# Performance work log

Hardware: AMD Instinct MI355X
Metric: run time of the kernel (lower is better)

Reference implementation:

```python
import jax, jax.numpy as jnp
import numpy as np

PD = 256            # pretrain_dim == dim_in (standard mode)
DZ = 128            # dim_z
PD2 = PD + 2        # feature dim after concatenating 2-d coords
FD = PD + 2 * PD2   # final_dim = 772
TEMP = float(DZ) ** 0.5
EPS = 1e-12
N1, N2 = 4096, 2048


def _lin_init(key, din, dout):
    w = jax.random.normal(key, (dout, din), jnp.float32) * 0.02
    b = jnp.zeros((dout,), jnp.float32)
    return w, b


def _lin(x, w, b):
    return x @ w.T + b


def setup_inputs() -> dict:
    key = jax.random.key(0)
    ks = jax.random.split(key, 13)
    lm_X = jax.random.normal(ks[0], (N1, PD), jnp.float32)
    lm_Y = jax.random.normal(ks[1], (N1, 2), jnp.float32)
    tg_X = jax.random.normal(ks[2], (N2, PD), jnp.float32)
    tg_Y = jax.random.normal(ks[3], (N2, 2), jnp.float32)
    lm_delay = jax.random.uniform(ks[4], (N1,), jnp.float32)
    tg_delay = jax.random.uniform(ks[5], (N2,), jnp.float32)
    aq_w, aq_b = _lin_init(ks[6], PD, DZ)    # att_attribute q proj
    ak_w, ak_b = _lin_init(ks[7], PD, DZ)    # att_attribute k proj
    w1_w, w1_b = _lin_init(ks[8], PD2, PD2)  # self.w_1
    w2_w, w2_b = _lin_init(ks[9], PD2, PD2)  # self.w_2
    pq_w, pq_b = _lin_init(ks[10], FD, DZ)   # pred attention q proj
    pk_w, pk_b = _lin_init(ks[11], PD, DZ)   # pred attention k proj
    pv_w, pv_b = _lin_init(ks[12], 2, 2)     # pred attention v proj
    gamma1 = jnp.ones((1, 1), jnp.float32)
    gamma2 = jnp.ones((1, 1), jnp.float32)
    gamma3 = jnp.ones((1, 1), jnp.float32)
    alpha = jnp.ones((1, 1), jnp.float32)
    beta = jnp.zeros((1, 1), jnp.float32)
    return dict(lm_X=lm_X, lm_Y=lm_Y, tg_X=tg_X, tg_Y=tg_Y,
                lm_delay=lm_delay, tg_delay=tg_delay,
                aq_w=aq_w, aq_b=aq_b, ak_w=ak_w, ak_b=ak_b,
                w1_w=w1_w, w1_b=w1_b, w2_w=w2_w, w2_b=w2_b,
                pq_w=pq_w, pq_b=pq_b, pk_w=pk_w, pk_b=pk_b,
                pv_w=pv_w, pv_b=pv_b,
                gamma1=gamma1, gamma2=gamma2, gamma3=gamma3,
                alpha=alpha, beta=beta)


def reference(lm_X, lm_Y, tg_X, tg_Y, lm_delay, tg_delay,
              aq_w, aq_b, ak_w, ak_b,
              w1_w, w1_b, w2_w, w2_b,
              pq_w, pq_b, pk_w, pk_b, pv_w, pv_b,
              gamma1, gamma2, gamma3, alpha, beta):
    n2 = tg_X.shape[0]
    a = alpha[0, 0]
    b0 = beta[0, 0]

    lm_feature = jnp.concatenate([lm_X, lm_Y], axis=1)            # [N1, PD2]
    tg_feature_0 = jnp.concatenate([tg_X, jnp.zeros((n2, 2), lm_X.dtype)], axis=1)
    router_0 = jnp.mean(lm_feature, axis=0)                        # [PD2]

    delay_score = jnp.exp(-gamma1[0, 0] * (a * lm_delay + b0))     # [N1]
    rou0 = jnp.exp(-gamma2[0, 0] * (a * tg_delay + b0))            # [N2]
    rou1 = jnp.exp(-gamma3[0, 0] * (a * tg_delay + b0))            # [N2]

    # SimpleAttention1: attribute score of targets over landmarks
    q = _lin(tg_X, aq_w, aq_b)
    k = _lin(lm_X, ak_w, ak_b)
    attr = jnp.exp(jax.nn.softmax((q / TEMP) @ k.T, axis=-1))      # [N2, N1]

    # Degree-normalized propagation of adj_matrix_0 (block-structured:
    # lm rows = identity, tg rows = [attr | I | rou0-col], router row = [delay | 0 | 1]).
    deg_tg0 = 1.0 + attr.sum(axis=1) + rou0                        # [N2]
    tg_prop0 = (attr @ lm_feature + tg_feature_0 + rou0[:, None] * router_0[None, :]) \
               / (deg_tg0 + EPS)[:, None]
    router_prop0 = (delay_score @ lm_feature + router_0) / (1.0 + delay_score.sum() + EPS)

    tg_feature_1 = _lin(tg_prop0, w1_w, w1_b)                      # [N2, PD2]
    router_1 = _lin(router_prop0[None, :], w1_w, w1_b)             # [1, PD2]

    # Second propagation: adj_matrix_1 = I + rou1 on tg->router column.
    tg_prop1 = (tg_feature_1 + rou1[:, None] * router_1) / (1.0 + rou1 + EPS)[:, None]
    tg_feature_2 = _lin(tg_prop1, w2_w, w2_b)                      # [N2, PD2]

    final_tg_feature = jnp.concatenate([tg_X, tg_feature_1, tg_feature_2], axis=-1)  # [N2, FD]

    # SimpleAttention2 (collaborative MLP prediction)
    q2 = _lin(final_tg_feature, pq_w, pq_b)
    k2 = _lin(lm_X, pk_w, pk_b)
    v2 = _lin(lm_Y, pv_w, pv_b)
    attn2 = jax.nn.softmax((q2 / TEMP) @ k2.T, axis=-1)            # [N2, N1]
    y_pred = attn2 @ v2                                            # [N2, 2]
    return y_pred, final_tg_feature
```

## Files before the change

kernel.cpp:

```cpp
#include <hip/hip_runtime.h>

#define N1 4096
#define N2 2048
#define PD 256
#define DZ 128
#define PD2 258
#define PD2P 264
#define FD 772
#define FDP 776
#define APN 272
#define APLD 72
#define SPLITS 16

typedef short s8v __attribute__((ext_vector_type(8)));
typedef float f32x4 __attribute__((ext_vector_type(4)));

__device__ __forceinline__ short f2b(float f) {
    union { float f; unsigned u; } v; v.f = f;
    unsigned r = v.u + 0x7fffu + ((v.u >> 16) & 1u);
    return (short)(r >> 16);
}
__device__ __forceinline__ float sb2f(short s) {
    union { unsigned u; float f; } v;
    v.u = ((unsigned)(unsigned short)s) << 16;
    return v.f;
}

constexpr int R0 = N2 * PD;
constexpr int R1 = R0 + PD2 * PD2P;
constexpr int R2 = R1 + PD2 * PD2P;
constexpr int R3 = R2 + DZ * FDP;
constexpr int R4 = R3 + APN * N1;
constexpr int R5 = R4 + 4096;
constexpr int R6 = R5 + 2048;
constexpr int R7 = R6 + N2 * 4;
constexpr int R8 = R7 + N2 * 6;

__global__ __launch_bounds__(256) void cvt_all(
    const float* __restrict__ lmX, const float* __restrict__ lmY,
    const float* __restrict__ tgX,
    const float* __restrict__ pqw, const float* __restrict__ w1w,
    const float* __restrict__ w2w,
    const float* __restrict__ lmd, const float* __restrict__ tgd,
    const float* __restrict__ g1, const float* __restrict__ g2,
    const float* __restrict__ g3, const float* __restrict__ al,
    const float* __restrict__ be,
    const float* __restrict__ pvw, const float* __restrict__ pvb,
    short* __restrict__ w1wb, short* __restrict__ w2wb,
    short* __restrict__ pqwb, short* __restrict__ lmFTb,
    float* __restrict__ dscore, float* __restrict__ rou0,
    float* __restrict__ rou1, float* __restrict__ v2b,
    float* __restrict__ Z, short* __restrict__ finalFb,
    short* __restrict__ tgp1b, float* __restrict__ outF)
{
    int i = blockIdx.x * 256 + threadIdx.x;
    if (i < R0) { int r = i >> 8, c = i & 255;
                  float v = tgX[i];
                  outF[(size_t)r * FD + c] = v;
                  finalFb[(size_t)r * FDP + c] = f2b(v); return; }
    if (i < R1) { int j = i - R0; int r = j / PD2P, c = j - r * PD2P;
                  w1wb[j] = (c < PD2) ? f2b(w1w[r * PD2 + c]) : (short)0; return; }
    if (i < R2) { int j = i - R1; int r = j / PD2P, c = j - r * PD2P;
                  w2wb[j] = (c < PD2) ? f2b(w2w[r * PD2 + c]) : (short)0; return; }
    if (i < R3) { int j = i - R2; int r = j / FDP, c = j - r * FDP;
                  pqwb[j] = (c < FD) ? f2b(pqw[r * FD + c]) : (short)0; return; }
    if (i < R4) { int j = i - R3; int c = j >> 12, r = j & (N1 - 1);
                  float v = 0.f;
                  if (c < PD) v = lmX[(size_t)r * PD + c];
                  else if (c < PD2) v = lmY[r * 2 + (c - PD)];
                  else if (c == PD2) v = 1.0f;
                  lmFTb[j] = f2b(v); return; }
    if (i < R5) { int j = i - R4;
                  float a = al[0], b = be[0];
                  dscore[j] = __expf(-g1[0] * (a * lmd[j] + b));
                  float y0 = lmY[2 * j], y1 = lmY[2 * j + 1];
                  v2b[2 * j]     = pvw[0] * y0 + pvw[1] * y1 + pvb[0];
                  v2b[2 * j + 1] = pvw[2] * y0 + pvw[3] * y1 + pvb[1];
                  if (j < N2) { float t = a * tgd[j] + b;
                                rou0[j] = __expf(-g2[0] * t);
                                rou1[j] = __expf(-g3[0] * t); }
                  return; }
    if (i < R6) { Z[i - R5] = 0.f; return; }
    if (i < R7) { int j = i - R6; int r = j >> 2;
                  finalFb[(size_t)r * FDP + FD + (j & 3)] = 0; return; }
    if (i < R8) { int j = i - R7; int r = j / 6;
                  tgp1b[(size_t)r * PD2P + PD2 + (j - r * 6)] = 0; return; }
}

__global__ __launch_bounds__(256) void rkq_kernel(
    const float* __restrict__ lmX, const float* __restrict__ tgX,
    const float* __restrict__ aqw, const float* __restrict__ aqb,
    const float* __restrict__ akw, const float* __restrict__ akb,
    const float* __restrict__ pkw, const float* __restrict__ pkb,
    const short* __restrict__ lmFTb, const float* __restrict__ dscore,
    float* __restrict__ router0, float* __restrict__ routerp0,
    short* __restrict__ kk, short* __restrict__ qb)
{
    __shared__ __align__(16) short LDS[5120];
    const int j = blockIdx.x, tid = threadIdx.x;
    const int lane = tid & 63, wv = tid >> 6;
    const int wm = wv >> 1, wn = wv & 1;
    const int lm = lane & 15, lq = lane >> 4;
    const f32x4 zero4 = {0.f, 0.f, 0.f, 0.f};

    if (j < 258) {
        float* r1 = (float*)LDS;
        float* r2 = r1 + 256;
        float* r3 = r2 + 256;
        const short* rowp = lmFTb + (size_t)j * N1;
        float s1 = 0.f, s2 = 0.f, s3 = 0.f;
        for (int i = tid; i < N1; i += 256) {
            float v = sb2f(rowp[i]);
            float d = dscore[i];
            s1 += v; s2 += d * v; s3 += d;
        }
        r1[tid] = s1; r2[tid] = s2; r3[tid] = s3; __syncthreads();
        for (int o = 128; o > 0; o >>= 1) {
            if (tid < o) { r1[tid] += r1[tid + o]; r2[tid] += r2[tid + o]; r3[tid] += r3[tid + o]; }
            __syncthreads();
        }
        if (tid == 0) {
            float r0v = r1[0] / (float)N1;
            router0[j] = r0v;
            routerp0[j] = (r2[0] + r0v) / (1.f + r3[0] + 1e-12f);
        }
        return;
    }
    short* Als = LDS;
    short* Bls = LDS + 64 * 40;
    f32x4 acc[2][2] = {{zero4, zero4}, {zero4, zero4}};
    const int r = tid >> 2, cgp = tid & 3;
    if (j < 514) {
        int jt = j - 258;
        int row0 = (jt >> 2) * 64, col0 = (jt & 3) * 64;
        for (int k0 = 0; k0 < 256; k0 += 32) {
            int gk = k0 + cgp * 8;
            const float* ap = lmX + (size_t)(row0 + r) * PD + gk;
            int c = col0 + r;
            const float* bp = (c < 128) ? akw + (size_t)c * PD + gk
                                        : pkw + (size_t)(c - 128) * PD + gk;
            s8v va, vb;
#pragma unroll
            for (int q = 0; q < 8; ++q) { va[q] = f2b(ap[q]); vb[q] = f2b(bp[q]); }
            *(s8v*)(Als + r * 40 + cgp * 8) = va;
            *(s8v*)(Bls + r * 40 + cgp * 8) = vb;
            __syncthreads();
            s8v af[2], bf[2];
#pragma unroll
            for (int mt = 0; mt < 2; ++mt)
                af[mt] = *(const s8v*)(Als + (wm * 32 + mt * 16 + lm) * 40 + lq * 8);
#pragma unroll
            for (int nt = 0; nt < 2; ++nt)
                bf[nt] = *(const s8v*)(Bls + (wn * 32 + nt * 16 + lm) * 40 + lq * 8);
#pragma unroll
            for (int mt = 0; mt < 2; ++mt)
#pragma unroll
                for (int nt = 0; nt < 2; ++nt)
                    acc[mt][nt] = __builtin_amdgcn_mfma_f32_16x16x32_bf16(
                        af[mt], bf[nt], acc[mt][nt], 0, 0, 0);
            __syncthreads();
        }
#pragma unroll
        for (int mt = 0; mt < 2; ++mt)
#pragma unroll
            for (int nt = 0; nt < 2; ++nt) {
                int c = col0 + wn * 32 + nt * 16 + lm;
                float bv = (c < 128) ? akb[c] : pkb[c - 128];
#pragma unroll
                for (int i = 0; i < 4; ++i) {
                    int rr = row0 + wm * 32 + mt * 16 + lq * 4 + i;
                    kk[(size_t)rr * 256 + c] = f2b(acc[mt][nt][i] + bv);
                }
            }
    } else {
        int jt = j - 514;
        int row0 = (jt >> 1) * 64, col0 = (jt & 1) * 64;
        for (int k0 = 0; k0 < 256; k0 += 32) {
            int gk = k0 + cgp * 8;
            const float* ap = tgX + (size_t)(row0 + r) * PD + gk;
            const float* bp = aqw + (size_t)(col0 + r) * PD + gk;
            s8v va, vb;
#pragma unroll
            for (int q = 0; q < 8; ++q) { va[q] = f2b(ap[q]); vb[q] = f2b(bp[q]); }
            *(s8v*)(Als + r * 40 + cgp * 8) = va;
            *(s8v*)(Bls + r * 40 + cgp * 8) = vb;
            __syncthreads();
            s8v af[2], bf[2];
#pragma unroll
            for (int mt = 0; mt < 2; ++mt)
                af[mt] = *(const s8v*)(Als + (wm * 32 + mt * 16 + lm) * 40 + lq * 8);
#pragma unroll
            for (int nt = 0; nt < 2; ++nt)
                bf[nt] = *(const s8v*)(Bls + (wn * 32 + nt * 16 + lm) * 40 + lq * 8);
#pragma unroll
            for (int mt = 0; mt < 2; ++mt)
#pragma unroll
                for (int nt = 0; nt < 2; ++nt)
                    acc[mt][nt] = __builtin_amdgcn_mfma_f32_16x16x32_bf16(
                        af[mt], bf[nt], acc[mt][nt], 0, 0, 0);
            __syncthreads();
        }
        const float INV_TEMP = 0.08838834764831845f;
#pragma unroll
        for (int mt = 0; mt < 2; ++mt)
#pragma unroll
            for (int nt = 0; nt < 2; ++nt) {
                int c = col0 + wn * 32 + nt * 16 + lm;
                float bv = aqb[c];
#pragma unroll
                for (int i = 0; i < 4; ++i) {
                    int rr = row0 + wm * 32 + mt * 16 + lq * 4 + i;
                    qb[(size_t)rr * DZ + c] = f2b(INV_TEMP * (acc[mt][nt][i] + bv));
                }
            }
    }
}

__global__ __launch_bounds__(256) void scores_e(
    const short* __restrict__ Q, const short* __restrict__ Kk,
    short* __restrict__ E, float* __restrict__ Z,
    const float* __restrict__ rp0, const float* __restrict__ w1w,
    const float* __restrict__ w1b, float* __restrict__ router1)
{
    const int j = blockIdx.x, tid = threadIdx.x;
    if (j == 512) {
        for (int c = tid; c < PD2; c += 256) {
            float s = w1b[c];
            const float* wr = w1w + (size_t)c * PD2;
            for (int k = 0; k < PD2; ++k) s += rp0[k] * wr[k];
            router1[c] = s;
        }
        return;
    }
    __shared__ __align__(16) short LDS[10240];
    short* Als = LDS;
    short* Bls = LDS + 128 * 40;
    const int lane = tid & 63, wv = tid >> 6;
    const int wm = wv >> 1, wn = wv & 1;
    const int lm = lane & 15, lq = lane >> 4;
    const int row0 = (j >> 5) * 128, col0 = (j & 31) * 128;
    const f32x4 zero4 = {0.f, 0.f, 0.f, 0.f};
    f32x4 acc[4][4];
#pragma unroll
    for (int mt = 0; mt < 4; ++mt)
#pragma unroll
        for (int nt = 0; nt < 4; ++nt) acc[mt][nt] = zero4;
    for (int k0 = 0; k0 < 128; k0 += 32) {
#pragma unroll
        for (int l = 0; l < 2; ++l) {
            int id = l * 256 + tid;
            int r = id >> 2, cgp = id & 3;
            int gk = k0 + cgp * 8;
            *(s8v*)(Als + r * 40 + cgp * 8) = *(const s8v*)(Q + (size_t)(row0 + r) * DZ + gk);
            *(s8v*)(Bls + r * 40 + cgp * 8) = *(const s8v*)(Kk + (size_t)(col0 + r) * 256 + gk);
        }
        __syncthreads();
        s8v af[4], bf[4];
#pragma unroll
        for (int mt = 0; mt < 4; ++mt)
            af[mt] = *(const s8v*)(Als + (wm * 64 + mt * 16 + lm) * 40 + lq * 8);
#pragma unroll
        for (int nt = 0; nt < 4; ++nt)
            bf[nt] = *(const s8v*)(Bls + (wn * 64 + nt * 16 + lm) * 40 + lq * 8);
#pragma unroll
        for (int mt = 0; mt < 4; ++mt)
#pragma unroll
            for (int nt = 0; nt < 4; ++nt)
                acc[mt][nt] = __builtin_amdgcn_mfma_f32_16x16x32_bf16(
                    af[mt], bf[nt], acc[mt][nt], 0, 0, 0);
        __syncthreads();
    }
#pragma unroll
    for (int mt = 0; mt < 4; ++mt)
#pragma unroll
        for (int i = 0; i < 4; ++i) {
            int r = row0 + wm * 64 + mt * 16 + lq * 4 + i;
            float rs = 0.f;
#pragma unroll
            for (int nt = 0; nt < 4; ++nt) {
                int c = col0 + wn * 64 + nt * 16 + lm;
                float e = __expf(acc[mt][nt][i]);
                E[(size_t)r * N1 + c] = f2b(e);
                rs += e;
            }
#pragma unroll
            for (int msk = 1; msk < 16; msk <<= 1) rs += __shfl_xor(rs, msk, 64);
            if (lm == 0) atomicAdd(&Z[r], rs);
        }
}

__global__ __launch_bounds__(512) void ap_gemm(const short* __restrict__ E,
                                               const float* __restrict__ Z,
                                               const short* __restrict__ lmFTb,
                                               short* __restrict__ part)
{
    __shared__ __align__(16) short LDS[28800];
    const int tid = threadIdx.x, bid = blockIdx.x;
    const int lane = tid & 63, w8 = tid >> 6;
    const int lm = lane & 15, lq = lane >> 4;
    const int s = bid & 15, row0 = (bid >> 4) * 128;
    const int kbase = s * (N1 / SPLITS);
    short* Als = LDS;
    short* Bls = LDS + 128 * APLD;
    const f32x4 zero4 = {0.f, 0.f, 0.f, 0.f};
    f32x4 acc[17];
#pragma unroll
    for (int nt = 0; nt < 17; ++nt) acc[nt] = zero4;
    for (int it = 0; it < (N1 / SPLITS) / 64; ++it) {
        int k0 = kbase + it * 64;
#pragma unroll
        for (int l = 0; l < 2; ++l) {
            int id = l * 512 + tid;
            int r = id >> 3, gg = id & 7;
            s8v ev = *(const s8v*)(E + (size_t)(row0 + r) * N1 + k0 + gg * 8);
            float invZ = __builtin_amdgcn_rcpf(Z[row0 + r]);
            s8v av;
#pragma unroll
            for (int q = 0; q < 8; ++q)
                av[q] = f2b(__expf(sb2f(ev[q]) * invZ));
            *(s8v*)(Als + r * APLD + gg * 8) = av;
        }
#pragma unroll
        for (int l = 0; l < 5; ++l) {
            int id = l * 512 + tid;
            if (id < APN * 8) {
                int r = id >> 3, gg = id & 7;
                *(s8v*)(Bls + r * APLD + gg * 8) =
                    *(const s8v*)(lmFTb + (size_t)r * N1 + k0 + gg * 8);
            }
        }
        __syncthreads();
        s8v a0 = *(const s8v*)(Als + (w8 * 16 + lm) * APLD + lq * 8);
        s8v a1 = *(const s8v*)(Als + (w8 * 16 + lm) * APLD + 32 + lq * 8);
#pragma unroll
        for (int nt = 0; nt < 17; ++nt) {
            s8v b0 = *(const s8v*)(Bls + (nt * 16 + lm) * APLD + lq * 8);
            s8v b1 = *(const s8v*)(Bls + (nt * 16 + lm) * APLD + 32 + lq * 8);
            acc[nt] = __builtin_amdgcn_mfma_f32_16x16x32_bf16(a0, b0, acc[nt], 0, 0, 0);
            acc[nt] = __builtin_amdgcn_mfma_f32_16x16x32_bf16(a1, b1, acc[nt], 0, 0, 0);
        }
        __syncthreads();
    }
    short* op = part + (size_t)s * N2 * APN;
#pragma unroll
    for (int nt = 0; nt < 17; ++nt) {
        int c = nt * 16 + lm;
#pragma unroll
        for (int i = 0; i < 4; ++i) {
            int r = row0 + w8 * 16 + lq * 4 + i;
            op[(size_t)r * APN + c] = f2b(acc[nt][i]);
        }
    }
}

__global__ __launch_bounds__(256) void fix_tgp0(const short* __restrict__ part,
                                                const float* __restrict__ tgX,
                                                const float* __restrict__ rou0,
                                                const float* __restrict__ router0,
                                                short* __restrict__ outb) {
    int r = blockIdx.x;
    int tid = threadIdx.x;
    __shared__ float sAsum;
    float s0 = 0.f, s1 = 0.f;
#pragma unroll
    for (int s = 0; s < SPLITS; ++s)
        s0 += sb2f(part[((size_t)s * N2 + r) * APN + tid]);
    if (tid < 8) {
#pragma unroll
        for (int s = 0; s < SPLITS; ++s)
            s1 += sb2f(part[((size_t)s * N2 + r) * APN + 256 + tid]);
    }
    if (tid == 2) sAsum = s1;
    __syncthreads();
    float ro = rou0[r];
    float inv = 1.f / (1.f + sAsum + ro + 1e-12f);
    {
        float v = (s0 + tgX[(size_t)r * PD + tid] + ro * router0[tid]) * inv;
        outb[(size_t)r * PD2P + tid] = f2b(v);
    }
    if (tid < 8) {
        int c = 256 + tid;
        float v = 0.f;
        if (c < PD2) v = (s1 + ro * router0[c]) * inv;
        outb[(size_t)r * PD2P + c] = f2b(v);
    }
}

__global__ __launch_bounds__(256) void w_gemm(
    const short* __restrict__ A, const short* __restrict__ B,
    const float* __restrict__ bias,
    float* __restrict__ outFcol, short* __restrict__ fFbcol,
    const float* __restrict__ rou1, const float* __restrict__ router1,
    short* __restrict__ tgp1b)
{
    __shared__ __align__(16) short LDS[5120];
    short* Als = LDS;
    short* Bls = LDS + 64 * 40;
    const int tid = threadIdx.x;
    const int lane = tid & 63, wv = tid >> 6;
    const int wm = wv >> 1, wn = wv & 1;
    const int lm = lane & 15, lq = lane >> 4;
    const int row0 = blockIdx.y * 64, col0 = blockIdx.x * 64;
    const f32x4 zero4 = {0.f, 0.f, 0.f, 0.f};
    f32x4 acc[2][2] = {{zero4, zero4}, {zero4, zero4}};
    const s8v zero8 = {0, 0, 0, 0, 0, 0, 0, 0};
    const int r = tid >> 2, cgp = tid & 3;
    for (int k0 = 0; k0 < PD2P; k0 += 32) {
        int gk = k0 + cgp * 8;
        s8v va = zero8, vb = zero8;
        if (gk < PD2P) {
            va = *(const s8v*)(A + (size_t)(row0 + r) * PD2P + gk);
            if (col0 + r < PD2) vb = *(const s8v*)(B + (size_t)(col0 + r) * PD2P + gk);
        }
        *(s8v*)(Als + r * 40 + cgp * 8) = va;
        *(s8v*)(Bls + r * 40 + cgp * 8) = vb;
        __syncthreads();
        s8v af[2], bf[2];
#pragma unroll
        for (int mt = 0; mt < 2; ++mt)
            af[mt] = *(const s8v*)(Als + (wm * 32 + mt * 16 + lm) * 40 + lq * 8);
#pragma unroll
        for (int nt = 0; nt < 2; ++nt)
            bf[nt] = *(const s8v*)(Bls + (wn * 32 + nt * 16 + lm) * 40 + lq * 8);
#pragma unroll
        for (int mt = 0; mt < 2; ++mt)
#pragma unroll
            for (int nt = 0; nt < 2; ++nt)
                acc[mt][nt] = __builtin_amdgcn_mfma_f32_16x16x32_bf16(
                    af[mt], bf[nt], acc[mt][nt], 0, 0, 0);
        __syncthreads();
    }
#pragma unroll
    for (int mt = 0; mt < 2; ++mt)
#pragma unroll
        for (int nt = 0; nt < 2; ++nt) {
            int c = col0 + wn * 32 + nt * 16 + lm;
            if (c >= PD2) continue;
            float bv = bias[c];
            float rc = router1 ? router1[c] : 0.f;
#pragma unroll
            for (int i = 0; i < 4; ++i) {
                int rr = row0 + wm * 32 + mt * 16 + lq * 4 + i;
                float v = acc[mt][nt][i] + bv;
                outFcol[(size_t)rr * FD + c] = v;
                fFbcol[(size_t)rr * FDP + c] = f2b(v);
                if (tgp1b) {
                    float ro = rou1[rr];
                    tgp1b[(size_t)rr * PD2P + c] =
                        f2b((v + ro * rc) / (1.f + ro + 1e-12f));
                }
            }
        }
}

__global__ __launch_bounds__(256) void q2_gemm(
    const short* __restrict__ A, const short* __restrict__ B,
    const float* __restrict__ bias, short* __restrict__ outB)
{
    __shared__ __align__(16) short LDS[5120];
    short* Als = LDS;
    short* Bls = LDS + 64 * 40;
    const int tid = threadIdx.x;
    const int lane = tid & 63, wv = tid >> 6;
    const int wm = wv >> 1, wn = wv & 1;
    const int lm = lane & 15, lq = lane >> 4;
    const int row0 = blockIdx.y * 64, col0 = blockIdx.x * 64;
    const f32x4 zero4 = {0.f, 0.f, 0.f, 0.f};
    f32x4 acc[2][2] = {{zero4, zero4}, {zero4, zero4}};
    const s8v zero8 = {0, 0, 0, 0, 0, 0, 0, 0};
    const int r = tid >> 2, cgp = tid & 3;
    for (int k0 = 0; k0 < FDP; k0 += 32) {
        int gk = k0 + cgp * 8;
        s8v va = zero8, vb = zero8;
        if (gk < FDP) {
            va = *(const s8v*)(A + (size_t)(row0 + r) * FDP + gk);
            vb = *(const s8v*)(B + (size_t)(col0 + r) * FDP + gk);
        }
        *(s8v*)(Als + r * 40 + cgp * 8) = va;
        *(s8v*)(Bls + r * 40 + cgp * 8) = vb;
        __syncthreads();
        s8v af[2], bf[2];
#pragma unroll
        for (int mt = 0; mt < 2; ++mt)
            af[mt] = *(const s8v*)(Als + (wm * 32 + mt * 16 + lm) * 40 + lq * 8);
#pragma unroll
        for (int nt = 0; nt < 2; ++nt)
            bf[nt] = *(const s8v*)(Bls + (wn * 32 + nt * 16 + lm) * 40 + lq * 8);
#pragma unroll
        for (int mt = 0; mt < 2; ++mt)
#pragma unroll
            for (int nt = 0; nt < 2; ++nt)
                acc[mt][nt] = __builtin_amdgcn_mfma_f32_16x16x32_bf16(
                    af[mt], bf[nt], acc[mt][nt], 0, 0, 0);
        __syncthreads();
    }
    const float INV_TEMP = 0.08838834764831845f;
#pragma unroll
    for (int mt = 0; mt < 2; ++mt)
#pragma unroll
        for (int nt = 0; nt < 2; ++nt) {
            int c = col0 + wn * 32 + nt * 16 + lm;
            float bv = bias[c];
#pragma unroll
            for (int i = 0; i < 4; ++i) {
                int rr = row0 + wm * 32 + mt * 16 + lq * 4 + i;
                outB[(size_t)rr * DZ + c] = f2b(INV_TEMP * (acc[mt][nt][i] + bv));
            }
        }
}

__global__ __launch_bounds__(256) void attn2_flash(
    const short* __restrict__ Q, const short* __restrict__ Kk,
    const float* __restrict__ V, float* __restrict__ part2,
    unsigned* __restrict__ done, float* __restrict__ out)
{
    __shared__ __align__(16) short Qls[64 * 136];
    __shared__ __align__(16) short Kls[64 * 136];
    __shared__ float Vls[128];
    __shared__ unsigned sdone;
    const int tid = threadIdx.x;
    const int lane = tid & 63, wv = tid >> 6;
    const int lm = lane & 15, lq = lane >> 4;
    const int chunk = blockIdx.x & 7, row0 = (blockIdx.x >> 3) * 64;
    const f32x4 zero4 = {0.f, 0.f, 0.f, 0.f};
#pragma unroll
    for (int l = 0; l < 4; ++l) {
        int id = l * 256 + tid;
        int r = id >> 4, g = id & 15;
        *(s8v*)(Qls + r * 136 + g * 8) = *(const s8v*)(Q + (size_t)(row0 + r) * DZ + g * 8);
    }
    __syncthreads();
    s8v af[4];
#pragma unroll
    for (int ks = 0; ks < 4; ++ks)
        af[ks] = *(const s8v*)(Qls + (wv * 16 + lm) * 136 + ks * 32 + lq * 8);
    float z[4] = {0.f, 0.f, 0.f, 0.f};
    float y0[4] = {0.f, 0.f, 0.f, 0.f};
    float y1[4] = {0.f, 0.f, 0.f, 0.f};
    for (int t = 0; t < 8; ++t) {
        int col0 = chunk * 512 + t * 64;
        __syncthreads();
#pragma unroll
        for (int l = 0; l < 4; ++l) {
            int id = l * 256 + tid;
            int r = id >> 4, g = id & 15;
            *(s8v*)(Kls + r * 136 + g * 8) =
                *(const s8v*)(Kk + (size_t)(col0 + r) * 256 + 128 + g * 8);
        }
        if (tid < 128) Vls[tid] = V[col0 * 2 + tid];
        __syncthreads();
        f32x4 acc[4];
#pragma unroll
        for (int nt = 0; nt < 4; ++nt) acc[nt] = zero4;
#pragma unroll
        for (int nt = 0; nt < 4; ++nt)
#pragma unroll
            for (int ks = 0; ks < 4; ++ks) {
                s8v bf = *(const s8v*)(Kls + (nt * 16 + lm) * 136 + ks * 32 + lq * 8);
                acc[nt] = __builtin_amdgcn_mfma_f32_16x16x32_bf16(af[ks], bf, acc[nt], 0, 0, 0);
            }
        float v0[4], v1[4];
#pragma unroll
        for (int nt = 0; nt < 4; ++nt) {
            v0[nt] = Vls[(nt * 16 + lm) * 2];
            v1[nt] = Vls[(nt * 16 + lm) * 2 + 1];
        }
#pragma unroll
        for (int i = 0; i < 4; ++i) {
            float e0 = __expf(acc[0][i]), e1 = __expf(acc[1][i]);
            float e2 = __expf(acc[2][i]), e3 = __expf(acc[3][i]);
            float pz = e0 + e1 + e2 + e3;
            float py0 = e0 * v0[0] + e1 * v0[1] + e2 * v0[2] + e3 * v0[3];
            float py1 = e0 * v1[0] + e1 * v1[1] + e2 * v1[2] + e3 * v1[3];
#pragma unroll
            for (int msk = 1; msk < 16; msk <<= 1) {
                pz  += __shfl_xor(pz, msk, 64);
                py0 += __shfl_xor(py0, msk, 64);
                py1 += __shfl_xor(py1, msk, 64);
            }
            z[i] += pz; y0[i] += py0; y1[i] += py1;
        }
    }
    if (lm == 0) {
#pragma unroll
        for (int i = 0; i < 4; ++i) {
            int r = row0 + wv * 16 + lq * 4 + i;
            float* pp = part2 + ((size_t)r * 8 + chunk) * 4;
            pp[0] = z[i]; pp[1] = y0[i]; pp[2] = y1[i];
        }
    }
    __threadfence();
    __syncthreads();
    if (tid == 0) sdone = atomicAdd(done, 1u);
    __syncthreads();
    if (sdone == 255u) {
        __threadfence();
        for (int r = tid; r < N2; r += 256) {
            const float* pp = part2 + (size_t)r * 32;
            float Zt = 0.f, Y0 = 0.f, Y1 = 0.f;
#pragma unroll
            for (int c = 0; c < 8; ++c) {
                Zt += pp[c * 4]; Y0 += pp[c * 4 + 1]; Y1 += pp[c * 4 + 2];
            }
            out[2 * r] = Y0 / Zt;
            out[2 * r + 1] = Y1 / Zt;
        }
    }
}

extern "C" void kernel_launch(void* const* d_in, const int* in_sizes, int n_in,
                              void* d_out, int out_size, void* d_ws, size_t ws_size,
                              hipStream_t stream) {
    const float* lm_X = (const float*)d_in[0];
    const float* lm_Y = (const float*)d_in[1];
    const float* tg_X = (const float*)d_in[2];
    const float* lm_delay = (const float*)d_in[4];
    const float* tg_delay = (const float*)d_in[5];
    const float* aq_w = (const float*)d_in[6];
    const float* aq_b = (const float*)d_in[7];
    const float* ak_w = (const float*)d_in[8];
    const float* ak_b = (const float*)d_in[9];
    const float* w1_w = (const float*)d_in[10];
    const float* w1_b = (const float*)d_in[11];
    const float* w2_w = (const float*)d_in[12];
    const float* w2_b = (const float*)d_in[13];
    const float* pq_w = (const float*)d_in[14];
    const float* pq_b = (const float*)d_in[15];
    const float* pk_w = (const float*)d_in[16];
    const float* pk_b = (const float*)d_in[17];
    const float* pv_w = (const float*)d_in[18];
    const float* pv_b = (const float*)d_in[19];
    const float* g1 = (const float*)d_in[20];
    const float* g2 = (const float*)d_in[21];
    const float* g3 = (const float*)d_in[22];
    const float* al = (const float*)d_in[23];
    const float* be = (const float*)d_in[24];

    float* out = (float*)d_out;
    float* outF = out + (size_t)N2 * 2;

    char* base = (char*)d_ws;
    size_t off = 0;
    auto allocF = [&](size_t n) -> float* {
        float* q = (float*)(base + off);
        off += (n * 4 + 255) / 256 * 256;
        return q;
    };
    auto allocS = [&](size_t n) -> short* {
        short* q = (short*)(base + off);
        off += (n * 2 + 255) / 256 * 256;
        return q;
    };

    short* E        = allocS((size_t)N2 * N1);
    short* appart   = allocS((size_t)SPLITS * N2 * APN);
    short* lmFTb    = allocS((size_t)APN * N1);
    short* qb       = allocS((size_t)N2 * DZ);
    short* kk       = allocS((size_t)N1 * 256);
    short* q2       = allocS((size_t)N2 * DZ);
    short* tgp0b    = allocS((size_t)N2 * PD2P);
    short* tgp1b    = allocS((size_t)N2 * PD2P);
    short* finalFb  = allocS((size_t)N2 * FDP);
    short* w1wb     = allocS((size_t)PD2 * PD2P);
    short* w2wb     = allocS((size_t)PD2 * PD2P);
    short* pqwb     = allocS((size_t)DZ * FDP);
    float* v2b      = allocF((size_t)N1 * 2);
    float* part2    = allocF((size_t)N2 * 32);
    float* Zbuf     = allocF(N2);
    float* router0  = allocF(PD2);
    float* routerp0 = allocF(PD2);
    float* router1  = allocF(PD2);
    float* dscore   = allocF(N1);
    float* rou0     = allocF(N2);
    float* rou1     = allocF(N2);
    unsigned* done  = (unsigned*)allocF(64);

    hipMemsetAsync(done, 0, 256, stream);

    hipLaunchKernelGGL(cvt_all, dim3((R8 + 255) / 256), dim3(256), 0, stream,
                       lm_X, lm_Y, tg_X, pq_w, w1_w, w2_w,
                       lm_delay, tg_delay, g1, g2, g3, al, be, pv_w, pv_b,
                       w1wb, w2wb, pqwb, lmFTb,
                       dscore, rou0, rou1, v2b, Zbuf, finalFb, tgp1b, outF);
    hipLaunchKernelGGL(rkq_kernel, dim3(578), dim3(256), 0, stream,
                       lm_X, tg_X, aq_w, aq_b, ak_w, ak_b, pk_w, pk_b,
                       lmFTb, dscore, router0, routerp0, kk, qb);
    hipLaunchKernelGGL(scores_e, dim3(513), dim3(256), 0, stream,
                       qb, kk, E, Zbuf, routerp0, w1_w, w1_b, router1);
    hipLaunchKernelGGL(ap_gemm, dim3(256), dim3(512), 0, stream, E, Zbuf, lmFTb, appart);
    hipLaunchKernelGGL(fix_tgp0, dim3(N2), dim3(256), 0, stream,
                       appart, tg_X, rou0, router0, tgp0b);
    hipLaunchKernelGGL(w_gemm, dim3(5, 32), dim3(256), 0, stream,
                       tgp0b, w1wb, w1_b, outF + 256, finalFb + 256, rou1, router1, tgp1b);
    hipLaunchKernelGGL(w_gemm, dim3(5, 32), dim3(256), 0, stream,
                       tgp1b, w2wb, w2_b, outF + 514, finalFb + 514,
                       nullptr, nullptr, nullptr);
    hipLaunchKernelGGL(q2_gemm, dim3(2, 32), dim3(256), 0, stream,
                       finalFb, pqwb, pq_b, q2);
    hipLaunchKernelGGL(attn2_flash, dim3(256), dim3(256), 0, stream,
                       q2, kk, v2b, part2, done, out);
}
```

Before: 253.5 us.

## Split attn2 across more column chunks and move combine to separate kernel

Doubles the column splits in the final attention from 8 to 16, launching 512 blocks that each cover 256 key columns, which raises occupancy on the GPU. The per-tile cross-lane shuffle reductions are deferred to a single reduction after the loop. The last-block atomic counter, threadfence and memset are replaced by a separate small combine kernel. This adds one kernel launch and doubles the partial-results buffer.

```diff
diff --git a/kernel.cpp b/kernel.cpp
--- a/kernel.cpp
+++ b/kernel.cpp
@@ -511,17 +511,15 @@
 
 __global__ __launch_bounds__(256) void attn2_flash(
     const short* __restrict__ Q, const short* __restrict__ Kk,
-    const float* __restrict__ V, float* __restrict__ part2,
-    unsigned* __restrict__ done, float* __restrict__ out)
+    const float* __restrict__ V, float* __restrict__ part2)
 {
     __shared__ __align__(16) short Qls[64 * 136];
     __shared__ __align__(16) short Kls[64 * 136];
     __shared__ float Vls[128];
-    __shared__ unsigned sdone;
     const int tid = threadIdx.x;
     const int lane = tid & 63, wv = tid >> 6;
     const int lm = lane & 15, lq = lane >> 4;
-    const int chunk = blockIdx.x & 7, row0 = (blockIdx.x >> 3) * 64;
+    const int chunk = blockIdx.x & 15, row0 = (blockIdx.x >> 4) * 64;
     const f32x4 zero4 = {0.f, 0.f, 0.f, 0.f};
 #pragma unroll
     for (int l = 0; l < 4; ++l) {
@@ -537,8 +535,8 @@
     float z[4] = {0.f, 0.f, 0.f, 0.f};
     float y0[4] = {0.f, 0.f, 0.f, 0.f};
     float y1[4] = {0.f, 0.f, 0.f, 0.f};
-    for (int t = 0; t < 8; ++t) {
-        int col0 = chunk * 512 + t * 64;
+    for (int t = 0; t < 4; ++t) {
+        int col0 = chunk * 256 + t * 64;
         __syncthreads();
 #pragma unroll
         for (int l = 0; l < 4; ++l) {
@@ -569,43 +567,41 @@
         for (int i = 0; i < 4; ++i) {
             float e0 = __expf(acc[0][i]), e1 = __expf(acc[1][i]);
             float e2 = __expf(acc[2][i]), e3 = __expf(acc[3][i]);
-            float pz = e0 + e1 + e2 + e3;
-            float py0 = e0 * v0[0] + e1 * v0[1] + e2 * v0[2] + e3 * v0[3];
-            float py1 = e0 * v1[0] + e1 * v1[1] + e2 * v1[2] + e3 * v1[3];
-#pragma unroll
-            for (int msk = 1; msk < 16; msk <<= 1) {
-                pz  += __shfl_xor(pz, msk, 64);
-                py0 += __shfl_xor(py0, msk, 64);
-                py1 += __shfl_xor(py1, msk, 64);
-            }
-            z[i] += pz; y0[i] += py0; y1[i] += py1;
+            z[i]  += e0 + e1 + e2 + e3;
+            y0[i] += e0 * v0[0] + e1 * v0[1] + e2 * v0[2] + e3 * v0[3];
+            y1[i] += e0 * v1[0] + e1 * v1[1] + e2 * v1[2] + e3 * v1[3];
+        }
+    }
+#pragma unroll
+    for (int i = 0; i < 4; ++i) {
+#pragma unroll
+        for (int msk = 1; msk < 16; msk <<= 1) {
+            z[i]  += __shfl_xor(z[i], msk, 64);
+            y0[i] += __shfl_xor(y0[i], msk, 64);
+            y1[i] += __shfl_xor(y1[i], msk, 64);
         }
     }
     if (lm == 0) {
 #pragma unroll
         for (int i = 0; i < 4; ++i) {
             int r = row0 + wv * 16 + lq * 4 + i;
-            float* pp = part2 + ((size_t)r * 8 + chunk) * 4;
+            float* pp = part2 + ((size_t)r * 16 + chunk) * 4;
             pp[0] = z[i]; pp[1] = y0[i]; pp[2] = y1[i];
         }
     }
-    __threadfence();
-    __syncthreads();
-    if (tid == 0) sdone = atomicAdd(done, 1u);
-    __syncthreads();
-    if (sdone == 255u) {
-        __threadfence();
-        for (int r = tid; r < N2; r += 256) {
-            const float* pp = part2 + (size_t)r * 32;
-            float Zt = 0.f, Y0 = 0.f, Y1 = 0.f;
-#pragma unroll
-            for (int c = 0; c < 8; ++c) {
-                Zt += pp[c * 4]; Y0 += pp[c * 4 + 1]; Y1 += pp[c * 4 + 2];
-            }
-            out[2 * r] = Y0 / Zt;
-            out[2 * r + 1] = Y1 / Zt;
-        }
-    }
+}
+
+__global__ void attn2_combine(const float* __restrict__ part2, float* __restrict__ out) {
+    int r = blockIdx.x * 256 + threadIdx.x;
+    if (r >= N2) return;
+    const float* pp = part2 + (size_t)r * 64;
+    float Zt = 0.f, Y0 = 0.f, Y1 = 0.f;
+#pragma unroll
+    for (int c = 0; c < 16; ++c) {
+        Zt += pp[c * 4]; Y0 += pp[c * 4 + 1]; Y1 += pp[c * 4 + 2];
+    }
+    out[2 * r] = Y0 / Zt;
+    out[2 * r + 1] = Y1 / Zt;
 }
 
 extern "C" void kernel_launch(void* const* d_in, const int* in_sizes, int n_in,
@@ -665,7 +661,7 @@
     short* w2wb     = allocS((size_t)PD2 * PD2P);
     short* pqwb     = allocS((size_t)DZ * FDP);
     float* v2b      = allocF((size_t)N1 * 2);
-    float* part2    = allocF((size_t)N2 * 32);
+    float* part2    = allocF((size_t)N2 * 64);
     float* Zbuf     = allocF(N2);
     float* router0  = allocF(PD2);
     float* routerp0 = allocF(PD2);
@@ -673,9 +669,6 @@
     float* dscore   = allocF(N1);
     float* rou0     = allocF(N2);
     float* rou1     = allocF(N2);
-    unsigned* done  = (unsigned*)allocF(64);
-
-    hipMemsetAsync(done, 0, 256, stream);
 
     hipLaunchKernelGGL(cvt_all, dim3((R8 + 255) / 256), dim3(256), 0, stream,
                        lm_X, lm_Y, tg_X, pq_w, w1_w, w2_w,
@@ -697,6 +690,7 @@
                        nullptr, nullptr, nullptr);
     hipLaunchKernelGGL(q2_gemm, dim3(2, 32), dim3(256), 0, stream,
                        finalFb, pqwb, pq_b, q2);
-    hipLaunchKernelGGL(attn2_flash, dim3(256), dim3(256), 0, stream,
-                       q2, kk, v2b, part2, done, out);
-}
+    hipLaunchKernelGGL(attn2_flash, dim3(512), dim3(256), 0, stream,
+                       q2, kk, v2b, part2);
+    hipLaunchKernelGGL(attn2_combine, dim3(8), dim3(256), 0, stream, part2, out);
+}
```

Measured after the change: 217.6 us. 14.1% less time.
